# Performance work log

Measured on AMD Instinct MI355X. Metric: run time of the kernel, lower is better.

## Reference

```python
import jax, jax.numpy as jnp
import numpy as np

T = 8          # timesteps (init arg T)
GAMA = 1.0     # ZIF surrogate width (init arg gama)
THRESH0 = 8.0  # initial scalar threshold (init arg thresh)

# ZIF spike function: heaviside forward, triangular surrogate backward
@jax.custom_vjp
def zif(v):
    return (v >= 0).astype(v.dtype)

def _zif_fwd(v):
    return (v >= 0).astype(v.dtype), v

def _zif_bwd(v, g):
    tmp = (1.0 / GAMA) * (1.0 / GAMA) * jnp.clip(GAMA - jnp.abs(v), 0.0)
    return (g * tmp,)

zif.defvjp(_zif_fwd, _zif_bwd)


def setup_inputs() -> dict:
    key = jax.random.key(0)
    k1, _ = jax.random.split(key)
    # pre-activation currents; scaled so a realistic fraction of neurons spike vs thresh=8
    x = jax.random.normal(k1, (T * 64, 128, 32, 32), dtype=jnp.float32) * 4.0 + 2.0
    thresh = jnp.full((1,), THRESH0, dtype=jnp.float32)
    return {"x": x, "thresh": thresh}


def reference(x, thresh):
    # self.thresh.data -> detached scalar threshold (adaptive thre is overridden by `current_thre = thre`)
    thre = jax.lax.stop_gradient(thresh)[0]
    B = x.shape[0] // T
    xs = x.reshape((T, B) + x.shape[1:])          # [T, B, C, H, W]

    mem0 = jnp.broadcast_to(0.5 * thre, xs.shape[1:]).astype(x.dtype)

    def step(mem, xt):
        mem = mem + xt
        spike = zif(mem - thre)
        mem = mem - spike * thre
        return mem, spike

    mem, spikes = jax.lax.scan(step, mem0, xs)     # mem: [B,C,H,W], spikes: [T,B,C,H,W]

    # final-step compensation / per-neuron effective threshold
    compen_mem = mem - 0.5 * thre
    spike_count = spikes.sum(axis=0)               # [B,C,H,W]
    compen_value = jnp.minimum(compen_mem + spike_count * thre, T * thre)
    cond = (compen_value > 0) & (spike_count > 0)
    safe_den = jnp.where(cond, spike_count, 1.0)
    new_thre = jnp.where(cond, compen_value / safe_den, 0.0)

    out = spikes * new_thre                        # broadcast over T
    return out.reshape((T * B,) + x.shape[1:])     # merge temporal dim
```

## Files before the change

### kernel.cpp

```cpp
#include <hip/hip_runtime.h>


typedef float f4 __attribute__((ext_vector_type(4)));
constexpr int T_STEPS = 8;
constexpr int COLS = 2;

__global__ __launch_bounds__(256) void newif_kernel(
    const f4* __restrict__ x, const float* __restrict__ thresh,
    f4* __restrict__ out, int n4)
{
    int base = blockIdx.x * (256 * COLS) + threadIdx.x;

    const float thre = thresh[0];
    const float half_thre = 0.5f * thre;
    const float tmax = 8.0f * thre;

    f4 xv[COLS][T_STEPS];
#pragma unroll
    for (int k = 0; k < COLS; ++k) {
        int col = base + k * 256;
#pragma unroll
        for (int t = 0; t < T_STEPS; ++t)
            xv[k][t] = x[t * n4 + col];
    }

#pragma unroll
    for (int k = 0; k < COLS; ++k) {
        f4 mem = {half_thre, half_thre, half_thre, half_thre};
        f4 cnt = {0.f, 0.f, 0.f, 0.f};
#pragma unroll
        for (int t = 0; t < T_STEPS; ++t) {
            mem += xv[k][t];
            f4 s;
            s.x = (mem.x >= thre) ? 1.0f : 0.0f;
            s.y = (mem.y >= thre) ? 1.0f : 0.0f;
            s.z = (mem.z >= thre) ? 1.0f : 0.0f;
            s.w = (mem.w >= thre) ? 1.0f : 0.0f;
            mem -= s * thre;
            cnt += s;
            xv[k][t] = s;
        }
        f4 nt;
#pragma unroll
        for (int c = 0; c < 4; ++c) {
            float mc = ((const float*)&mem)[c];
            float cc = ((const float*)&cnt)[c];
            float compen_value = fminf((mc - half_thre) + cc * thre, tmax);
            bool cond = (compen_value > 0.0f) && (cc > 0.0f);
            ((float*)&nt)[c] = cond ? (compen_value / cc) : 0.0f;
        }
        int col = base + k * 256;
#pragma unroll
        for (int t = 0; t < T_STEPS; ++t)
            __builtin_nontemporal_store(xv[k][t] * nt, &out[t * n4 + col]);
    }
}

extern "C" void kernel_launch(void* const* d_in, const int* in_sizes, int n_in,
                              void* d_out, int out_size, void* d_ws, size_t ws_size,
                              hipStream_t stream) {
    const float* x      = (const float*)d_in[0];
    const float* thresh = (const float*)d_in[1];
    float* out          = (float*)d_out;

    int n_total = in_sizes[0];
    int n4      = n_total / T_STEPS / 4;

    const int block = 256;
    int grid = n4 / (block * COLS);
    newif_kernel<<<grid, block, 0, stream>>>(
        (const f4*)x, thresh, (f4*)out, n4);
}
```

Baseline: 459.8 us.

## Split LIF into scan kernel writing spike bitmask plus expand kernel

Replaces the single fused kernel with two kernels. The first runs the temporal scan and writes a per-neuron threshold plus an 8-bit spike mask to workspace. The second reads these and expands them into the T output planes. A single-column fused fallback is kept for when the workspace is too small. This adds extra global traffic and a second launch over a workload that was already bandwidth-bound, presumably to reduce register pressure and get a cleaner store stream.

```diff
diff --git a/kernel.cpp b/kernel.cpp
--- a/kernel.cpp
+++ b/kernel.cpp
@@ -3,57 +3,140 @@
 
 typedef float f4 __attribute__((ext_vector_type(4)));
 constexpr int T_STEPS = 8;
-constexpr int COLS = 2;
 
-__global__ __launch_bounds__(256) void newif_kernel(
+__global__ __launch_bounds__(256) void newif_scan(
     const f4* __restrict__ x, const float* __restrict__ thresh,
-    f4* __restrict__ out, int n4)
+    f4* __restrict__ thre_out, uchar4* __restrict__ mask_out, int n4)
 {
-    int base = blockIdx.x * (256 * COLS) + threadIdx.x;
+    int i = blockIdx.x * 256 + threadIdx.x;
+    if (i >= n4) return;
 
     const float thre = thresh[0];
     const float half_thre = 0.5f * thre;
     const float tmax = 8.0f * thre;
 
-    f4 xv[COLS][T_STEPS];
-#pragma unroll
-    for (int k = 0; k < COLS; ++k) {
-        int col = base + k * 256;
-#pragma unroll
-        for (int t = 0; t < T_STEPS; ++t)
-            xv[k][t] = x[t * n4 + col];
+    const f4* xp = x + i;
+    f4 x0 = xp[0 * n4], x1 = xp[1 * n4], x2 = xp[2 * n4], x3 = xp[3 * n4];
+    f4 x4 = xp[4 * n4], x5 = xp[5 * n4], x6 = xp[6 * n4], x7 = xp[7 * n4];
+
+    float m0 = half_thre, m1 = half_thre, m2 = half_thre, m3 = half_thre;
+    float c0 = 0.f, c1 = 0.f, c2 = 0.f, c3 = 0.f;
+    unsigned k0 = 0u, k1 = 0u, k2 = 0u, k3 = 0u;
+
+#define STEP(xv, t)                                         \
+    {                                                       \
+        m0 += xv.x; m1 += xv.y; m2 += xv.z; m3 += xv.w;     \
+        float s0 = (m0 >= thre) ? 1.0f : 0.0f;              \
+        float s1 = (m1 >= thre) ? 1.0f : 0.0f;              \
+        float s2 = (m2 >= thre) ? 1.0f : 0.0f;              \
+        float s3 = (m3 >= thre) ? 1.0f : 0.0f;              \
+        m0 -= s0 * thre; c0 += s0;                          \
+        m1 -= s1 * thre; c1 += s1;                          \
+        m2 -= s2 * thre; c2 += s2;                          \
+        m3 -= s3 * thre; c3 += s3;                          \
+        k0 |= (m0 != m0 + 0.f, (s0 != 0.f) ? (1u << t) : 0u); \
+        k1 |= (s1 != 0.f) ? (1u << t) : 0u;                 \
+        k2 |= (s2 != 0.f) ? (1u << t) : 0u;                 \
+        k3 |= (s3 != 0.f) ? (1u << t) : 0u;                 \
+    }
+#undef STEP
+#define STEP(xv, t)                                         \
+    {                                                       \
+        m0 += xv.x; m1 += xv.y; m2 += xv.z; m3 += xv.w;     \
+        float s0 = (m0 >= thre) ? 1.0f : 0.0f;              \
+        float s1 = (m1 >= thre) ? 1.0f : 0.0f;              \
+        float s2 = (m2 >= thre) ? 1.0f : 0.0f;              \
+        float s3 = (m3 >= thre) ? 1.0f : 0.0f;              \
+        m0 -= s0 * thre; c0 += s0;                          \
+        m1 -= s1 * thre; c1 += s1;                          \
+        m2 -= s2 * thre; c2 += s2;                          \
+        m3 -= s3 * thre; c3 += s3;                          \
+        if (s0 != 0.f) k0 |= (1u << t);                     \
+        if (s1 != 0.f) k1 |= (1u << t);                     \
+        if (s2 != 0.f) k2 |= (1u << t);                     \
+        if (s3 != 0.f) k3 |= (1u << t);                     \
     }
 
+    STEP(x0, 0) STEP(x1, 1) STEP(x2, 2) STEP(x3, 3)
+    STEP(x4, 4) STEP(x5, 5) STEP(x6, 6) STEP(x7, 7)
+#undef STEP
+
+    f4 nt;
+#define NEWTHRE(mc, cc, dst)                                            \
+    {                                                                   \
+        float compen_value = fminf((mc - half_thre) + cc * thre, tmax); \
+        bool cond = (compen_value > 0.0f) && (cc > 0.0f);               \
+        dst = cond ? (compen_value / cc) : 0.0f;                        \
+    }
+    NEWTHRE(m0, c0, nt.x)
+    NEWTHRE(m1, c1, nt.y)
+    NEWTHRE(m2, c2, nt.z)
+    NEWTHRE(m3, c3, nt.w)
+#undef NEWTHRE
+
+    thre_out[i] = nt;
+    mask_out[i] = make_uchar4((unsigned char)k0, (unsigned char)k1,
+                              (unsigned char)k2, (unsigned char)k3);
+}
+
+__global__ __launch_bounds__(256) void newif_expand(
+    const f4* __restrict__ thre_in, const uchar4* __restrict__ mask_in,
+    f4* __restrict__ out, int n4)
+{
+    int i = blockIdx.x * 256 + threadIdx.x;
+    if (i >= n4) return;
+
+    f4 nt = thre_in[i];
+    uchar4 mk = mask_in[i];
+    f4* op = out + i;
+
 #pragma unroll
-    for (int k = 0; k < COLS; ++k) {
-        f4 mem = {half_thre, half_thre, half_thre, half_thre};
-        f4 cnt = {0.f, 0.f, 0.f, 0.f};
+    for (int t = 0; t < T_STEPS; ++t) {
+        f4 o;
+        o.x = ((mk.x >> t) & 1) ? nt.x : 0.0f;
+        o.y = ((mk.y >> t) & 1) ? nt.y : 0.0f;
+        o.z = ((mk.z >> t) & 1) ? nt.z : 0.0f;
+        o.w = ((mk.w >> t) & 1) ? nt.w : 0.0f;
+        __builtin_nontemporal_store(o, op + t * n4);
+    }
+}
+
+__global__ __launch_bounds__(256) void newif_fused(
+    const f4* __restrict__ x, const float* __restrict__ thresh,
+    f4* __restrict__ out, int n4)
+{
+    int i = blockIdx.x * 256 + threadIdx.x;
+    if (i >= n4) return;
+    const float thre = thresh[0];
+    const float half_thre = 0.5f * thre;
+    const float tmax = 8.0f * thre;
+    const f4* xp = x + i;
+    f4 xs[T_STEPS];
 #pragma unroll
-        for (int t = 0; t < T_STEPS; ++t) {
-            mem += xv[k][t];
-            f4 s;
-            s.x = (mem.x >= thre) ? 1.0f : 0.0f;
-            s.y = (mem.y >= thre) ? 1.0f : 0.0f;
-            s.z = (mem.z >= thre) ? 1.0f : 0.0f;
-            s.w = (mem.w >= thre) ? 1.0f : 0.0f;
-            mem -= s * thre;
-            cnt += s;
-            xv[k][t] = s;
-        }
-        f4 nt;
+    for (int t = 0; t < T_STEPS; ++t) xs[t] = xp[t * n4];
+    f4 mem = {half_thre, half_thre, half_thre, half_thre};
+    f4 cnt = {0.f, 0.f, 0.f, 0.f};
 #pragma unroll
-        for (int c = 0; c < 4; ++c) {
-            float mc = ((const float*)&mem)[c];
-            float cc = ((const float*)&cnt)[c];
-            float compen_value = fminf((mc - half_thre) + cc * thre, tmax);
-            bool cond = (compen_value > 0.0f) && (cc > 0.0f);
-            ((float*)&nt)[c] = cond ? (compen_value / cc) : 0.0f;
-        }
-        int col = base + k * 256;
+    for (int t = 0; t < T_STEPS; ++t) {
+        mem += xs[t];
+        f4 s;
+        s.x = (mem.x >= thre) ? 1.0f : 0.0f;
+        s.y = (mem.y >= thre) ? 1.0f : 0.0f;
+        s.z = (mem.z >= thre) ? 1.0f : 0.0f;
+        s.w = (mem.w >= thre) ? 1.0f : 0.0f;
+        mem -= s * thre; cnt += s; xs[t] = s;
+    }
+    f4 nt;
 #pragma unroll
-        for (int t = 0; t < T_STEPS; ++t)
-            __builtin_nontemporal_store(xv[k][t] * nt, &out[t * n4 + col]);
+    for (int c = 0; c < 4; ++c) {
+        float mc = ((const float*)&mem)[c], cc = ((const float*)&cnt)[c];
+        float cv = fminf((mc - half_thre) + cc * thre, tmax);
+        ((float*)&nt)[c] = ((cv > 0.f) && (cc > 0.f)) ? (cv / cc) : 0.0f;
     }
+    f4* op = out + i;
+#pragma unroll
+    for (int t = 0; t < T_STEPS; ++t)
+        __builtin_nontemporal_store(xs[t] * nt, op + t * n4);
 }
 
 extern "C" void kernel_launch(void* const* d_in, const int* in_sizes, int n_in,
@@ -67,7 +150,19 @@
     int n4      = n_total / T_STEPS / 4;
 
     const int block = 256;
-    int grid = n4 / (block * COLS);
-    newif_kernel<<<grid, block, 0, stream>>>(
-        (const f4*)x, thresh, (f4*)out, n4);
+    int grid = (n4 + block - 1) / block;
+
+    size_t thre_bytes = (size_t)n4 * 16;
+    size_t mask_bytes = (size_t)n4 * 4;
+    if (ws_size >= thre_bytes + mask_bytes) {
+        f4* thre_ws     = (f4*)d_ws;
+        uchar4* mask_ws = (uchar4*)((char*)d_ws + thre_bytes);
+        newif_scan<<<grid, block, 0, stream>>>(
+            (const f4*)x, thresh, thre_ws, mask_ws, n4);
+        newif_expand<<<grid, block, 0, stream>>>(
+            (const f4*)thre_ws, (const uchar4*)mask_ws, (f4*)out, n4);
+    } else {
+        newif_fused<<<grid, block, 0, stream>>>(
+            (const f4*)x, thresh, (f4*)out, n4);
+    }
 }
```

Result: no change. 457.8 us (-0.4%).
